# Optimization experiments

Hardware: AMD Instinct MI355X
Metric: run time of the kernel (lower is better)

Reference implementation:

```python
import jax, jax.numpy as jnp
import numpy as np

N_NODES = 100000
N_EDGES = 1600000
D_FEAT = 128


def setup_inputs() -> dict:
    key = jax.random.key(0)
    k1, k2, k3 = jax.random.split(key, 3)
    feat = jax.random.normal(k1, (N_NODES, D_FEAT), dtype=jnp.float32)
    src = jax.random.randint(k2, (N_EDGES,), 0, N_NODES, dtype=jnp.int32)
    dst = jax.random.randint(k3, (N_EDGES,), 0, N_NODES, dtype=jnp.int32)
    return {"feat": feat, "src": src, "dst": dst}


def reference(feat, src, dst):
    n = feat.shape[0]
    ones = jnp.ones(src.shape[0], dtype=feat.dtype)
    # out-degree of each node (as message source), clamped to >= 1
    deg_o = jnp.clip(jax.ops.segment_sum(ones, src, num_segments=n), 1.0)
    norm_l = deg_o ** -0.5  # [N]
    feat_scaled = feat * norm_l[:, None]
    # copy_u + sum aggregation: gather from src, scatter-add to dst
    agg = jax.ops.segment_sum(feat_scaled[src], dst, num_segments=n)
    # in-degree normalization on destination side
    deg_i = jnp.clip(jax.ops.segment_sum(ones, dst, num_segments=n), 1.0)
    norm_r = deg_i ** -0.5
    return agg * norm_r[:, None]
```

## Files before the change

### kernel.cpp

```cpp
#include <hip/hip_runtime.h>
#include <hip/hip_fp16.h>

#define D_FEAT      128
#define SCAN_B      1024
#define S_BIN       512
#define BUCKET_BITS 7
#define BUCKET_SZ   128
#define NB_MAX      1024
#define SORT_CAP    6144

typedef float f32x4 __attribute__((ext_vector_type(4)));

__global__ void binhist2_kernel(const int* __restrict__ src, const int* __restrict__ dst,
                                int* __restrict__ part2, int n_edges, int nb, int N2,
                                int slice_len) {
    __shared__ int hd[NB_MAX];
    __shared__ int hs[NB_MAX];
    int s = blockIdx.x;
    for (int i = threadIdx.x; i < nb; i += blockDim.x) { hd[i] = 0; hs[i] = 0; }
    __syncthreads();
    int beg = s * slice_len;
    int end = beg + slice_len; if (end > n_edges) end = n_edges;
    for (int i = beg + threadIdx.x; i < end; i += blockDim.x) {
        atomicAdd(&hd[dst[i] >> BUCKET_BITS], 1);
        atomicAdd(&hs[src[i] >> BUCKET_BITS], 1);
    }
    __syncthreads();
    for (int b = threadIdx.x; b < nb; b += blockDim.x) {
        part2[(size_t)b * S_BIN + s] = hd[b];
        part2[(size_t)(N2 + b * S_BIN) + s] = hs[b];
    }
}

__global__ __launch_bounds__(SCAN_B) void scan1_kernel(int* __restrict__ data,
        int* __restrict__ bsum, int n) {
    __shared__ int sh[SCAN_B];
    int t = threadIdx.x;
    int g = blockIdx.x * SCAN_B + t;
    int v = (g < n) ? data[g] : 0;
    sh[t] = v;
    __syncthreads();
    for (int d = 1; d < SCAN_B; d <<= 1) {
        int x = (t >= d) ? sh[t - d] : 0;
        __syncthreads();
        sh[t] += x;
        __syncthreads();
    }
    if (g < n) data[g] = sh[t] - v;
    if (t == SCAN_B - 1) bsum[blockIdx.x] = sh[t];
}

__global__ __launch_bounds__(SCAN_B) void scan2_kernel(int* __restrict__ bsum, int nb) {
    __shared__ int sh[SCAN_B];
    int t = threadIdx.x;
    int v = (t < nb) ? bsum[t] : 0;
    sh[t] = v;
    __syncthreads();
    for (int d = 1; d < SCAN_B; d <<= 1) {
        int x = (t >= d) ? sh[t - d] : 0;
        __syncthreads();
        sh[t] += x;
        __syncthreads();
    }
    if (t < nb) bsum[t] = sh[t] - v;
}

__global__ void binscatter2_kernel(const int* __restrict__ src, const int* __restrict__ dst,
                                   const int* __restrict__ loff, const int* __restrict__ bsum,
                                   int* __restrict__ colp, unsigned char* __restrict__ colp_src,
                                   int n_edges, int nb, int N2, int slice_len) {
    __shared__ int cd[NB_MAX];
    __shared__ int cs[NB_MAX];
    int s = blockIdx.x;
    for (int b = threadIdx.x; b < nb; b += blockDim.x) {
        size_t iD = (size_t)b * S_BIN + s;
        size_t iS = (size_t)N2 + (size_t)b * S_BIN + s;
        cd[b] = loff[iD] + bsum[iD >> 10];
        cs[b] = loff[iS] + bsum[iS >> 10] - n_edges;
    }
    __syncthreads();
    int beg = s * slice_len;
    int end = beg + slice_len; if (end > n_edges) end = n_edges;
    for (int i = beg + threadIdx.x; i < end; i += blockDim.x) {
        int d = dst[i], sv = src[i];
        int pD = atomicAdd(&cd[d >> BUCKET_BITS], 1);
        colp[pD] = sv | ((d & (BUCKET_SZ - 1)) << 20);
        int pS = atomicAdd(&cs[sv >> BUCKET_BITS], 1);
        colp_src[pS] = (unsigned char)(sv & (BUCKET_SZ - 1));
    }
}

__global__ __launch_bounds__(256) void sortcount_kernel(
        int* __restrict__ colp, const unsigned char* __restrict__ colp_src,
        const int* __restrict__ loff, const int* __restrict__ bsum,
        int* __restrict__ node_off, float* __restrict__ norm_l,
        int n_nodes, int n_edges, int nb, int N2) {
    __shared__ int buf[SORT_CAP];
    __shared__ int cnt[BUCKET_SZ];
    __shared__ int sa[BUCKET_SZ];
    __shared__ int sb[BUCKET_SZ];
    int tid = threadIdx.x;

    if ((int)blockIdx.x >= nb) {
        int b = blockIdx.x - nb;
        size_t iA = (size_t)N2 + (size_t)b * S_BIN;
        int beg = loff[iA] + bsum[iA >> 10] - n_edges;
        int end;
        if (b + 1 < nb) {
            size_t iB = (size_t)N2 + (size_t)(b + 1) * S_BIN;
            end = loff[iB] + bsum[iB >> 10] - n_edges;
        } else end = n_edges;
        if (tid < BUCKET_SZ) cnt[tid] = 0;
        __syncthreads();
        for (int i = beg + tid; i < end; i += blockDim.x)
            atomicAdd(&cnt[colp_src[i]], 1);
        __syncthreads();
        int node0 = b << BUCKET_BITS;
        int bn = n_nodes - node0; if (bn > BUCKET_SZ) bn = BUCKET_SZ;
        if (tid < bn) {
            int c = cnt[tid]; if (c < 1) c = 1;
            norm_l[node0 + tid] = rsqrtf((float)c);
        }
        return;
    }

    int b = blockIdx.x;
    size_t iA = (size_t)b * S_BIN;
    int beg = loff[iA] + bsum[iA >> 10];
    int end;
    if (b + 1 < nb) {
        size_t iB = (size_t)(b + 1) * S_BIN;
        end = loff[iB] + bsum[iB >> 10];
    } else end = n_edges;
    int m = end - beg;
    if (tid < BUCKET_SZ) cnt[tid] = 0;
    __syncthreads();
    for (int i = tid; i < m; i += blockDim.x) {
        int v = colp[beg + i];
        if (i < SORT_CAP) buf[i] = v;
        atomicAdd(&cnt[(v >> 20) & (BUCKET_SZ - 1)], 1);
    }
    __syncthreads();
    int* rp = sa; int* wp = sb;
    if (tid < BUCKET_SZ) sa[tid] = cnt[tid];
    __syncthreads();
    for (int d = 1; d < BUCKET_SZ; d <<= 1) {
        if (tid < BUCKET_SZ) wp[tid] = rp[tid] + (tid >= d ? rp[tid - d] : 0);
        __syncthreads();
        int* t = rp; rp = wp; wp = t;
    }
    int node0 = b << BUCKET_BITS;
    int bn = n_nodes - node0; if (bn > BUCKET_SZ) bn = BUCKET_SZ;
    if (tid < BUCKET_SZ) {
        int ex = rp[tid] - cnt[tid];
        wp[tid] = ex;
        if (tid < bn) node_off[node0 + tid] = beg + ex;
    }
    if (b == nb - 1 && tid == 0) node_off[n_nodes] = end;
    __syncthreads();
    int mm = m < SORT_CAP ? m : SORT_CAP;
    for (int i = tid; i < mm; i += blockDim.x) {
        int v = buf[i];
        int p = atomicAdd(&wp[(v >> 20) & (BUCKET_SZ - 1)], 1);
        colp[beg + p] = v & 0xFFFFF;
    }
}

__global__ void convert_kernel(const float* __restrict__ feat, const float* __restrict__ norm_l,
                               __half* __restrict__ feat16, int n_nodes) {
    int t = blockIdx.x * blockDim.x + threadIdx.x;
    int total = n_nodes * (D_FEAT / 8);
    if (t >= total) return;
    float nl = norm_l[t >> 4];
    const f32x4* fp = (const f32x4*)feat + (size_t)t * 2;
    f32x4 a = __builtin_nontemporal_load(fp);
    f32x4 b = __builtin_nontemporal_load(fp + 1);
    __half2 h0 = __floats2half2_rn(a.x * nl, a.y * nl);
    __half2 h1 = __floats2half2_rn(a.z * nl, a.w * nl);
    __half2 h2 = __floats2half2_rn(b.x * nl, b.y * nl);
    __half2 h3 = __floats2half2_rn(b.z * nl, b.w * nl);
    uint4 o;
    o.x = *(unsigned int*)&h0; o.y = *(unsigned int*)&h1;
    o.z = *(unsigned int*)&h2; o.w = *(unsigned int*)&h3;
    ((uint4*)feat16)[t] = o;
}

__global__ __launch_bounds__(256) void pull_csr_kernel(
        const __half* __restrict__ feat16, const int* __restrict__ col,
        const int* __restrict__ node_off, float* __restrict__ out, int n_nodes) {
    int lane = threadIdx.x & 63;
    int wid  = (int)(((long long)blockIdx.x * blockDim.x + threadIdx.x) >> 6);
    int h  = lane >> 5;
    int g  = (lane >> 4) & 1;
    int dl = lane & 15;
    int node = wid * 2 + h;
    bool nvalid = node < n_nodes;
    int nsafe = nvalid ? node : n_nodes - 1;
    int s = node_off[nsafe];
    int e = nvalid ? node_off[nsafe + 1] : s;
    int m = e - s;
    int om = __shfl_xor(m, 32, 64);
    int mm = m > om ? m : om;

    float a0=0.f,a1=0.f,a2=0.f,a3=0.f,a4=0.f,a5=0.f,a6=0.f,a7=0.f;
    const uint4* rowb = (const uint4*)feat16;

    for (int base = 0; base < mm; base += 32) {
        int remh = m - base;
        int cl = lane & 31;
        int ci = cl;
        if (ci >= remh) ci = (remh > 0) ? remh - 1 : 0;
        int cv = col[s + base + ci];
        int lim = mm - base; if (lim > 32) lim = 32;
        for (int k = 0; k < lim; k += 2) {
            int srcl = (lane & 32) + k + g;
            int idx = __shfl(cv, srcl, 64);
            if (base + k + g < m) {
                uint4 hv = rowb[((size_t)(unsigned)idx << 4) + dl];
                float2 f;
                f = __half22float2(*(__half2*)&hv.x); a0 += f.x; a1 += f.y;
                f = __half22float2(*(__half2*)&hv.y); a2 += f.x; a3 += f.y;
                f = __half22float2(*(__half2*)&hv.z); a4 += f.x; a5 += f.y;
                f = __half22float2(*(__half2*)&hv.w); a6 += f.x; a7 += f.y;
            }
        }
    }

    a0 += __shfl_xor(a0, 16, 64); a1 += __shfl_xor(a1, 16, 64);
    a2 += __shfl_xor(a2, 16, 64); a3 += __shfl_xor(a3, 16, 64);
    a4 += __shfl_xor(a4, 16, 64); a5 += __shfl_xor(a5, 16, 64);
    a6 += __shfl_xor(a6, 16, 64); a7 += __shfl_xor(a7, 16, 64);

    if (nvalid && g == 0) {
        int c = m < 1 ? 1 : m;
        float nr = rsqrtf((float)c);
        f32x4 o0 = {a0 * nr, a1 * nr, a2 * nr, a3 * nr};
        f32x4 o1 = {a4 * nr, a5 * nr, a6 * nr, a7 * nr};
        f32x4* op = (f32x4*)(out + (size_t)node * D_FEAT) + dl * 2;
        __builtin_nontemporal_store(o0, op);
        __builtin_nontemporal_store(o1, op + 1);
    }
}

extern "C" void kernel_launch(void* const* d_in, const int* in_sizes, int n_in,
                              void* d_out, int out_size, void* d_ws, size_t ws_size,
                              hipStream_t stream) {
    const float* feat = (const float*)d_in[0];
    const int*   src  = (const int*)d_in[1];
    const int*   dst  = (const int*)d_in[2];
    float* out = (float*)d_out;

    const int n_nodes = in_sizes[0] / D_FEAT;
    const int n_edges = in_sizes[1];
    const int nb = (n_nodes + BUCKET_SZ - 1) / BUCKET_SZ;
    const int N2 = nb * S_BIN;
    const int NSCAN = 2 * N2;
    const int sl = (n_edges + S_BIN - 1) / S_BIN;

    auto alignup = [](size_t x) { return (x + 255) & ~(size_t)255; };
    char* p = (char*)d_ws;
    int*    node_off = (int*)p;            p += alignup((size_t)(n_nodes + 1) * 4);
    float*  norm_l   = (float*)p;          p += alignup((size_t)n_nodes * 4);
    int*    part2    = (int*)p;            p += alignup((size_t)NSCAN * 4);
    int*    bsum     = (int*)p;            p += alignup((size_t)SCAN_B * 4);
    int*    colp     = (int*)p;            p += alignup((size_t)n_edges * 4);
    unsigned char* colp_src = (unsigned char*)p; p += alignup((size_t)n_edges);
    __half* feat16   = (__half*)p;

    binhist2_kernel<<<S_BIN, 256, 0, stream>>>(src, dst, part2, n_edges, nb, N2, sl);

    {
        int nsb = (NSCAN + SCAN_B - 1) / SCAN_B;
        scan1_kernel<<<nsb, SCAN_B, 0, stream>>>(part2, bsum, NSCAN);
        scan2_kernel<<<1, SCAN_B, 0, stream>>>(bsum, nsb);
    }

    binscatter2_kernel<<<S_BIN, 256, 0, stream>>>(src, dst, part2, bsum, colp, colp_src,
                                                  n_edges, nb, N2, sl);

    sortcount_kernel<<<2 * nb, 256, 0, stream>>>(colp, colp_src, part2, bsum, node_off,
                                                 norm_l, n_nodes, n_edges, nb, N2);

    {
        int total = n_nodes * (D_FEAT / 8);
        convert_kernel<<<(total + 255) / 256, 256, 0, stream>>>(feat, norm_l, feat16, n_nodes);
    }

    {
        long long waves = ((long long)n_nodes + 1) / 2;
        long long total = waves * 64;
        pull_csr_kernel<<<(int)((total + 255) / 256), 256, 0, stream>>>(feat16, colp, node_off,
                                                                        out, n_nodes);
    }
}
```

Before: 248.7 us.

## Fuse CSR preprocessing phases into one cooperative kernel with grid syncs

Merges the histogram, two-level scan, bin-scatter, per-bucket sort/count and fp16 conversion kernels into a single cooperative launch of 256 blocks of 1024 threads, separated by grid.sync. The intent is to remove per-kernel launch overhead and the idle gaps between the small preprocessing kernels. The edge slicing drops from 512 to 256 slices with 1024 threads each, and a multi-kernel fallback runs if the cooperative launch fails. The pull kernel's gather is also made branch-free by clamping column indices and multiplying by a 0/1 mask. The risks are grid-sync cost, lower occupancy from 1024-thread blocks, and wasted loads for masked edges.

```diff
diff --git a/kernel.cpp b/kernel.cpp
--- a/kernel.cpp
+++ b/kernel.cpp
@@ -1,108 +1,107 @@
 #include <hip/hip_runtime.h>
 #include <hip/hip_fp16.h>
+#include <hip/hip_cooperative_groups.h>
+
+namespace cg = cooperative_groups;
 
 #define D_FEAT      128
-#define SCAN_B      1024
-#define S_BIN       512
+#define S_BIN       256
 #define BUCKET_BITS 7
 #define BUCKET_SZ   128
 #define NB_MAX      1024
 #define SORT_CAP    6144
+#define CTHREADS    1024
+#define CGRID       256
+#define SMEM_INTS   6528
 
 typedef float f32x4 __attribute__((ext_vector_type(4)));
 
-__global__ void binhist2_kernel(const int* __restrict__ src, const int* __restrict__ dst,
-                                int* __restrict__ part2, int n_edges, int nb, int N2,
-                                int slice_len) {
-    __shared__ int hd[NB_MAX];
-    __shared__ int hs[NB_MAX];
-    int s = blockIdx.x;
-    for (int i = threadIdx.x; i < nb; i += blockDim.x) { hd[i] = 0; hs[i] = 0; }
-    __syncthreads();
-    int beg = s * slice_len;
-    int end = beg + slice_len; if (end > n_edges) end = n_edges;
-    for (int i = beg + threadIdx.x; i < end; i += blockDim.x) {
+
+__device__ void ph_binhist(int* sm, const int* __restrict__ src, const int* __restrict__ dst,
+                           int* __restrict__ part2, int n_edges, int nb, int N2,
+                           int s, int sl, int tid, int nthr) {
+    int* hd = sm; int* hs = sm + NB_MAX;
+    for (int i = tid; i < nb; i += nthr) { hd[i] = 0; hs[i] = 0; }
+    __syncthreads();
+    int beg = s * sl;
+    int end = beg + sl; if (end > n_edges) end = n_edges;
+    for (int i = beg + tid; i < end; i += nthr) {
         atomicAdd(&hd[dst[i] >> BUCKET_BITS], 1);
         atomicAdd(&hs[src[i] >> BUCKET_BITS], 1);
     }
     __syncthreads();
-    for (int b = threadIdx.x; b < nb; b += blockDim.x) {
+    for (int b = tid; b < nb; b += nthr) {
         part2[(size_t)b * S_BIN + s] = hd[b];
         part2[(size_t)(N2 + b * S_BIN) + s] = hs[b];
     }
 }
 
-__global__ __launch_bounds__(SCAN_B) void scan1_kernel(int* __restrict__ data,
-        int* __restrict__ bsum, int n) {
-    __shared__ int sh[SCAN_B];
-    int t = threadIdx.x;
-    int g = blockIdx.x * SCAN_B + t;
+__device__ void ph_scan_chunk(int* sm, int* __restrict__ data, int* __restrict__ bsum,
+                              int n, int chunk, int tid) {
+    int g = chunk * CTHREADS + tid;
     int v = (g < n) ? data[g] : 0;
-    sh[t] = v;
-    __syncthreads();
-    for (int d = 1; d < SCAN_B; d <<= 1) {
-        int x = (t >= d) ? sh[t - d] : 0;
-        __syncthreads();
-        sh[t] += x;
-        __syncthreads();
-    }
-    if (g < n) data[g] = sh[t] - v;
-    if (t == SCAN_B - 1) bsum[blockIdx.x] = sh[t];
-}
-
-__global__ __launch_bounds__(SCAN_B) void scan2_kernel(int* __restrict__ bsum, int nb) {
-    __shared__ int sh[SCAN_B];
-    int t = threadIdx.x;
-    int v = (t < nb) ? bsum[t] : 0;
-    sh[t] = v;
-    __syncthreads();
-    for (int d = 1; d < SCAN_B; d <<= 1) {
-        int x = (t >= d) ? sh[t - d] : 0;
-        __syncthreads();
-        sh[t] += x;
-        __syncthreads();
-    }
-    if (t < nb) bsum[t] = sh[t] - v;
-}
-
-__global__ void binscatter2_kernel(const int* __restrict__ src, const int* __restrict__ dst,
-                                   const int* __restrict__ loff, const int* __restrict__ bsum,
-                                   int* __restrict__ colp, unsigned char* __restrict__ colp_src,
-                                   int n_edges, int nb, int N2, int slice_len) {
-    __shared__ int cd[NB_MAX];
-    __shared__ int cs[NB_MAX];
-    int s = blockIdx.x;
-    for (int b = threadIdx.x; b < nb; b += blockDim.x) {
+    sm[tid] = v;
+    __syncthreads();
+    for (int d = 1; d < CTHREADS; d <<= 1) {
+        int x = (tid >= d) ? sm[tid - d] : 0;
+        __syncthreads();
+        sm[tid] += x;
+        __syncthreads();
+    }
+    if (g < n) data[g] = sm[tid] - v;
+    if (tid == CTHREADS - 1) bsum[chunk] = sm[tid];
+}
+
+__device__ void ph_scan_top(int* sm, int* __restrict__ bsum, int nchunks, int tid) {
+    int v = (tid < nchunks) ? bsum[tid] : 0;
+    sm[tid] = v;
+    __syncthreads();
+    for (int d = 1; d < CTHREADS; d <<= 1) {
+        int x = (tid >= d) ? sm[tid - d] : 0;
+        __syncthreads();
+        sm[tid] += x;
+        __syncthreads();
+    }
+    if (tid < nchunks) bsum[tid] = sm[tid] - v;
+}
+
+__device__ void ph_binscatter(int* sm, const int* __restrict__ src, const int* __restrict__ dst,
+                              const int* __restrict__ loff, const int* __restrict__ bsum,
+                              int* __restrict__ colp, unsigned char* __restrict__ colp_src,
+                              int n_edges, int nb, int N2, int s, int sl, int tid, int nthr) {
+    int* cd = sm; int* cs = sm + NB_MAX;
+    for (int b = tid; b < nb; b += nthr) {
         size_t iD = (size_t)b * S_BIN + s;
         size_t iS = (size_t)N2 + (size_t)b * S_BIN + s;
         cd[b] = loff[iD] + bsum[iD >> 10];
         cs[b] = loff[iS] + bsum[iS >> 10] - n_edges;
     }
     __syncthreads();
-    int beg = s * slice_len;
-    int end = beg + slice_len; if (end > n_edges) end = n_edges;
-    for (int i = beg + threadIdx.x; i < end; i += blockDim.x) {
+    int beg = s * sl;
+    int end = beg + sl; if (end > n_edges) end = n_edges;
+    for (int i = beg + tid; i < end; i += nthr) {
         int d = dst[i], sv = src[i];
         int pD = atomicAdd(&cd[d >> BUCKET_BITS], 1);
         colp[pD] = sv | ((d & (BUCKET_SZ - 1)) << 20);
         int pS = atomicAdd(&cs[sv >> BUCKET_BITS], 1);
         colp_src[pS] = (unsigned char)(sv & (BUCKET_SZ - 1));
     }
-}
-
-__global__ __launch_bounds__(256) void sortcount_kernel(
-        int* __restrict__ colp, const unsigned char* __restrict__ colp_src,
-        const int* __restrict__ loff, const int* __restrict__ bsum,
-        int* __restrict__ node_off, float* __restrict__ norm_l,
-        int n_nodes, int n_edges, int nb, int N2) {
-    __shared__ int buf[SORT_CAP];
-    __shared__ int cnt[BUCKET_SZ];
-    __shared__ int sa[BUCKET_SZ];
-    __shared__ int sb[BUCKET_SZ];
-    int tid = threadIdx.x;
-
-    if ((int)blockIdx.x >= nb) {
-        int b = blockIdx.x - nb;
+    __syncthreads();
+}
+
+__device__ void ph_sortunit(int* sm, int* __restrict__ colp,
+                            const unsigned char* __restrict__ colp_src,
+                            const int* __restrict__ loff, const int* __restrict__ bsum,
+                            int* __restrict__ node_off, float* __restrict__ norm_l,
+                            int n_nodes, int n_edges, int nb, int N2, int u, int tid, int nthr) {
+    int* buf = sm;
+    int* cnt = sm + SORT_CAP;
+    int* sa  = sm + SORT_CAP + BUCKET_SZ;
+    int* sb  = sm + SORT_CAP + 2 * BUCKET_SZ;
+    __syncthreads();
+
+    if (u >= nb) {
+        int b = u - nb;
         size_t iA = (size_t)N2 + (size_t)b * S_BIN;
         int beg = loff[iA] + bsum[iA >> 10] - n_edges;
         int end;
@@ -112,7 +111,7 @@
         } else end = n_edges;
         if (tid < BUCKET_SZ) cnt[tid] = 0;
         __syncthreads();
-        for (int i = beg + tid; i < end; i += blockDim.x)
+        for (int i = beg + tid; i < end; i += nthr)
             atomicAdd(&cnt[colp_src[i]], 1);
         __syncthreads();
         int node0 = b << BUCKET_BITS;
@@ -121,10 +120,11 @@
             int c = cnt[tid]; if (c < 1) c = 1;
             norm_l[node0 + tid] = rsqrtf((float)c);
         }
+        __syncthreads();
         return;
     }
 
-    int b = blockIdx.x;
+    int b = u;
     size_t iA = (size_t)b * S_BIN;
     int beg = loff[iA] + bsum[iA >> 10];
     int end;
@@ -135,7 +135,7 @@
     int m = end - beg;
     if (tid < BUCKET_SZ) cnt[tid] = 0;
     __syncthreads();
-    for (int i = tid; i < m; i += blockDim.x) {
+    for (int i = tid; i < m; i += nthr) {
         int v = colp[beg + i];
         if (i < SORT_CAP) buf[i] = v;
         atomicAdd(&cnt[(v >> 20) & (BUCKET_SZ - 1)], 1);
@@ -159,35 +159,103 @@
     if (b == nb - 1 && tid == 0) node_off[n_nodes] = end;
     __syncthreads();
     int mm = m < SORT_CAP ? m : SORT_CAP;
-    for (int i = tid; i < mm; i += blockDim.x) {
+    for (int i = tid; i < mm; i += nthr) {
         int v = buf[i];
         int p = atomicAdd(&wp[(v >> 20) & (BUCKET_SZ - 1)], 1);
         colp[beg + p] = v & 0xFFFFF;
     }
-}
-
-__global__ void convert_kernel(const float* __restrict__ feat, const float* __restrict__ norm_l,
-                               __half* __restrict__ feat16, int n_nodes) {
-    int t = blockIdx.x * blockDim.x + threadIdx.x;
-    int total = n_nodes * (D_FEAT / 8);
-    if (t >= total) return;
-    float nl = norm_l[t >> 4];
-    const f32x4* fp = (const f32x4*)feat + (size_t)t * 2;
-    f32x4 a = __builtin_nontemporal_load(fp);
-    f32x4 b = __builtin_nontemporal_load(fp + 1);
-    __half2 h0 = __floats2half2_rn(a.x * nl, a.y * nl);
-    __half2 h1 = __floats2half2_rn(a.z * nl, a.w * nl);
-    __half2 h2 = __floats2half2_rn(b.x * nl, b.y * nl);
-    __half2 h3 = __floats2half2_rn(b.z * nl, b.w * nl);
-    uint4 o;
-    o.x = *(unsigned int*)&h0; o.y = *(unsigned int*)&h1;
-    o.z = *(unsigned int*)&h2; o.w = *(unsigned int*)&h3;
-    ((uint4*)feat16)[t] = o;
+    __syncthreads();
+}
+
+__device__ void ph_convert(const float* __restrict__ feat, const float* __restrict__ norm_l,
+                           __half* __restrict__ feat16, int total, int gid, int stride) {
+    for (int t = gid; t < total; t += stride) {
+        float nl = norm_l[t >> 4];
+        const f32x4* fp = (const f32x4*)feat + (size_t)t * 2;
+        f32x4 a = __builtin_nontemporal_load(fp);
+        f32x4 b = __builtin_nontemporal_load(fp + 1);
+        __half2 h0 = __floats2half2_rn(a.x * nl, a.y * nl);
+        __half2 h1 = __floats2half2_rn(a.z * nl, a.w * nl);
+        __half2 h2 = __floats2half2_rn(b.x * nl, b.y * nl);
+        __half2 h3 = __floats2half2_rn(b.z * nl, b.w * nl);
+        uint4 o;
+        o.x = *(unsigned int*)&h0; o.y = *(unsigned int*)&h1;
+        o.z = *(unsigned int*)&h2; o.w = *(unsigned int*)&h3;
+        ((uint4*)feat16)[t] = o;
+    }
+}
+
+
+__global__ __launch_bounds__(CTHREADS) void coop_preproc(
+        const int* __restrict__ src, const int* __restrict__ dst,
+        const float* __restrict__ feat, int* __restrict__ part2, int* __restrict__ bsum,
+        int* __restrict__ colp, unsigned char* __restrict__ colp_src,
+        int* __restrict__ node_off, float* __restrict__ norm_l, __half* __restrict__ feat16,
+        int n_nodes, int n_edges, int nb, int N2, int sl) {
+    __shared__ int sm[SMEM_INTS];
+    cg::grid_group grid = cg::this_grid();
+    int tid = threadIdx.x, blk = blockIdx.x;
+    int NSCAN = 2 * N2;
+    int nch = (NSCAN + CTHREADS - 1) / CTHREADS;
+
+    ph_binhist(sm, src, dst, part2, n_edges, nb, N2, blk, sl, tid, CTHREADS);
+    grid.sync();
+    for (int c = blk; c < nch; c += CGRID) {
+        __syncthreads();
+        ph_scan_chunk(sm, part2, bsum, NSCAN, c, tid);
+    }
+    grid.sync();
+    if (blk == 0) ph_scan_top(sm, bsum, nch, tid);
+    grid.sync();
+    ph_binscatter(sm, src, dst, part2, bsum, colp, colp_src, n_edges, nb, N2, blk, sl,
+                  tid, CTHREADS);
+    grid.sync();
+    for (int u = blk; u < 2 * nb; u += CGRID)
+        ph_sortunit(sm, colp, colp_src, part2, bsum, node_off, norm_l,
+                    n_nodes, n_edges, nb, N2, u, tid, CTHREADS);
+    grid.sync();
+    ph_convert(feat, norm_l, feat16, n_nodes * (D_FEAT / 8),
+               blk * CTHREADS + tid, CGRID * CTHREADS);
+}
+
+
+__global__ __launch_bounds__(CTHREADS) void k_binhist(const int* src, const int* dst, int* part2,
+        int n_edges, int nb, int N2, int sl) {
+    __shared__ int sm[SMEM_INTS];
+    ph_binhist(sm, src, dst, part2, n_edges, nb, N2, blockIdx.x, sl, threadIdx.x, CTHREADS);
+}
+__global__ __launch_bounds__(CTHREADS) void k_scan1(int* data, int* bsum, int n) {
+    __shared__ int sm[SMEM_INTS];
+    ph_scan_chunk(sm, data, bsum, n, blockIdx.x, threadIdx.x);
+}
+__global__ __launch_bounds__(CTHREADS) void k_scan2(int* bsum, int nchunks) {
+    __shared__ int sm[SMEM_INTS];
+    ph_scan_top(sm, bsum, nchunks, threadIdx.x);
+}
+__global__ __launch_bounds__(CTHREADS) void k_binscatter(const int* src, const int* dst,
+        const int* loff, const int* bsum, int* colp, unsigned char* colp_src,
+        int n_edges, int nb, int N2, int sl) {
+    __shared__ int sm[SMEM_INTS];
+    ph_binscatter(sm, src, dst, loff, bsum, colp, colp_src, n_edges, nb, N2, blockIdx.x, sl,
+                  threadIdx.x, CTHREADS);
+}
+__global__ __launch_bounds__(CTHREADS) void k_sortcount(int* colp, const unsigned char* colp_src,
+        const int* loff, const int* bsum, int* node_off, float* norm_l,
+        int n_nodes, int n_edges, int nb, int N2) {
+    __shared__ int sm[SMEM_INTS];
+    ph_sortunit(sm, colp, colp_src, loff, bsum, node_off, norm_l, n_nodes, n_edges, nb, N2,
+                blockIdx.x, threadIdx.x, CTHREADS);
+}
+__global__ __launch_bounds__(CTHREADS) void k_convert(const float* feat, const float* norm_l,
+        __half* feat16, int total) {
+    ph_convert(feat, norm_l, feat16, total,
+               blockIdx.x * blockDim.x + threadIdx.x, gridDim.x * blockDim.x);
 }
 
 __global__ __launch_bounds__(256) void pull_csr_kernel(
         const __half* __restrict__ feat16, const int* __restrict__ col,
-        const int* __restrict__ node_off, float* __restrict__ out, int n_nodes) {
+        const int* __restrict__ node_off, float* __restrict__ out,
+        int n_nodes, int n_edges) {
     int lane = threadIdx.x & 63;
     int wid  = (int)(((long long)blockIdx.x * blockDim.x + threadIdx.x) >> 6);
     int h  = lane >> 5;
@@ -207,22 +275,22 @@
 
     for (int base = 0; base < mm; base += 32) {
         int remh = m - base;
-        int cl = lane & 31;
-        int ci = cl;
+        int ci = lane & 31;
         if (ci >= remh) ci = (remh > 0) ? remh - 1 : 0;
-        int cv = col[s + base + ci];
+        int cidx = s + base + ci;
+        if (cidx >= n_edges) cidx = n_edges - 1;
+        int cv = col[cidx];
         int lim = mm - base; if (lim > 32) lim = 32;
         for (int k = 0; k < lim; k += 2) {
             int srcl = (lane & 32) + k + g;
             int idx = __shfl(cv, srcl, 64);
-            if (base + k + g < m) {
-                uint4 hv = rowb[((size_t)(unsigned)idx << 4) + dl];
-                float2 f;
-                f = __half22float2(*(__half2*)&hv.x); a0 += f.x; a1 += f.y;
-                f = __half22float2(*(__half2*)&hv.y); a2 += f.x; a3 += f.y;
-                f = __half22float2(*(__half2*)&hv.z); a4 += f.x; a5 += f.y;
-                f = __half22float2(*(__half2*)&hv.w); a6 += f.x; a7 += f.y;
-            }
+            uint4 hv = rowb[((size_t)(unsigned)idx << 4) + dl];
+            float wm = (base + k + g < m) ? 1.f : 0.f;
+            float2 f;
+            f = __half22float2(*(__half2*)&hv.x); a0 += wm * f.x; a1 += wm * f.y;
+            f = __half22float2(*(__half2*)&hv.y); a2 += wm * f.x; a3 += wm * f.y;
+            f = __half22float2(*(__half2*)&hv.z); a4 += wm * f.x; a5 += wm * f.y;
+            f = __half22float2(*(__half2*)&hv.w); a6 += wm * f.x; a7 += wm * f.y;
         }
     }
 
@@ -250,46 +318,48 @@
     const int*   dst  = (const int*)d_in[2];
     float* out = (float*)d_out;
 
-    const int n_nodes = in_sizes[0] / D_FEAT;
-    const int n_edges = in_sizes[1];
-    const int nb = (n_nodes + BUCKET_SZ - 1) / BUCKET_SZ;
-    const int N2 = nb * S_BIN;
-    const int NSCAN = 2 * N2;
-    const int sl = (n_edges + S_BIN - 1) / S_BIN;
+    int n_nodes = in_sizes[0] / D_FEAT;
+    int n_edges = in_sizes[1];
+    int nb = (n_nodes + BUCKET_SZ - 1) / BUCKET_SZ;
+    int N2 = nb * S_BIN;
+    int NSCAN = 2 * N2;
+    int sl = (n_edges + S_BIN - 1) / S_BIN;
 
     auto alignup = [](size_t x) { return (x + 255) & ~(size_t)255; };
     char* p = (char*)d_ws;
     int*    node_off = (int*)p;            p += alignup((size_t)(n_nodes + 1) * 4);
     float*  norm_l   = (float*)p;          p += alignup((size_t)n_nodes * 4);
     int*    part2    = (int*)p;            p += alignup((size_t)NSCAN * 4);
-    int*    bsum     = (int*)p;            p += alignup((size_t)SCAN_B * 4);
+    int*    bsum     = (int*)p;            p += alignup((size_t)CTHREADS * 4);
     int*    colp     = (int*)p;            p += alignup((size_t)n_edges * 4);
     unsigned char* colp_src = (unsigned char*)p; p += alignup((size_t)n_edges);
     __half* feat16   = (__half*)p;
 
-    binhist2_kernel<<<S_BIN, 256, 0, stream>>>(src, dst, part2, n_edges, nb, N2, sl);
-
-    {
-        int nsb = (NSCAN + SCAN_B - 1) / SCAN_B;
-        scan1_kernel<<<nsb, SCAN_B, 0, stream>>>(part2, bsum, NSCAN);
-        scan2_kernel<<<1, SCAN_B, 0, stream>>>(bsum, nsb);
-    }
-
-    binscatter2_kernel<<<S_BIN, 256, 0, stream>>>(src, dst, part2, bsum, colp, colp_src,
-                                                  n_edges, nb, N2, sl);
-
-    sortcount_kernel<<<2 * nb, 256, 0, stream>>>(colp, colp_src, part2, bsum, node_off,
-                                                 norm_l, n_nodes, n_edges, nb, N2);
-
-    {
-        int total = n_nodes * (D_FEAT / 8);
-        convert_kernel<<<(total + 255) / 256, 256, 0, stream>>>(feat, norm_l, feat16, n_nodes);
+    void* cargs[] = { (void*)&src, (void*)&dst, (void*)&feat, (void*)&part2, (void*)&bsum,
+                      (void*)&colp, (void*)&colp_src, (void*)&node_off, (void*)&norm_l,
+                      (void*)&feat16, (void*)&n_nodes, (void*)&n_edges, (void*)&nb,
+                      (void*)&N2, (void*)&sl };
+    hipError_t cerr = hipLaunchCooperativeKernel((const void*)coop_preproc,
+                                                 dim3(CGRID), dim3(CTHREADS),
+                                                 cargs, 0, stream);
+    if (cerr != hipSuccess) {
+        int nch = (NSCAN + CTHREADS - 1) / CTHREADS;
+        k_binhist<<<S_BIN, CTHREADS, 0, stream>>>(src, dst, part2, n_edges, nb, N2, sl);
+        k_scan1<<<nch, CTHREADS, 0, stream>>>(part2, bsum, NSCAN);
+        k_scan2<<<1, CTHREADS, 0, stream>>>(bsum, nch);
+        k_binscatter<<<S_BIN, CTHREADS, 0, stream>>>(src, dst, part2, bsum, colp, colp_src,
+                                                     n_edges, nb, N2, sl);
+        k_sortcount<<<2 * nb, CTHREADS, 0, stream>>>(colp, colp_src, part2, bsum, node_off,
+                                                     norm_l, n_nodes, n_edges, nb, N2);
+        int total16 = n_nodes * (D_FEAT / 8);
+        k_convert<<<(total16 + CTHREADS - 1) / CTHREADS, CTHREADS, 0, stream>>>(
+            feat, norm_l, feat16, total16);
     }
 
     {
         long long waves = ((long long)n_nodes + 1) / 2;
         long long total = waves * 64;
         pull_csr_kernel<<<(int)((total + 255) / 256), 256, 0, stream>>>(feat16, colp, node_off,
-                                                                        out, n_nodes);
-    }
-}
+                                                                        out, n_nodes, n_edges);
+    }
+}
```

Result: slower. 398.8 us (+60.3%).
